# Kernel optimization log

Hardware: AMD Instinct MI355X
Metric: run time of the kernel (lower is better)

The kernel has to match this reference:

```python
import jax, jax.numpy as jnp
import numpy as np

N, E, F_IN, H, C = 10000, 320000, 256, 256, 40


def setup_inputs() -> dict:
    key = jax.random.key(0)
    ks = jax.random.split(key, 12)
    inp = {
        "x": jax.random.normal(ks[0], (N, F_IN), dtype=jnp.float32),
        "edge_index": jax.random.randint(ks[1], (2, E), 0, N, dtype=jnp.int64),
    }
    dims = [(F_IN, H), (H, H), (H, H), (H, H), (H, C)]
    for i, (din, dout) in enumerate(dims, start=1):
        scale = 1.0 / np.sqrt(din)
        inp[f"W{i}"] = jax.random.normal(ks[1 + i], (din, dout), dtype=jnp.float32) * scale
        inp[f"b{i}"] = jnp.zeros((dout,), dtype=jnp.float32)
    return inp


def _gcn_norm(edge_index, num_nodes, dtype):
    # GCNConv: add self-loops, symmetric normalization D^-1/2 (A+I) D^-1/2
    loops = jnp.arange(num_nodes, dtype=edge_index.dtype)
    src = jnp.concatenate([edge_index[0], loops])
    dst = jnp.concatenate([edge_index[1], loops])
    deg = jax.ops.segment_sum(jnp.ones_like(dst, dtype=dtype), dst, num_segments=num_nodes)
    dinv = jnp.where(deg > 0, deg ** -0.5, 0.0).astype(dtype)
    norm = dinv[src] * dinv[dst]  # [E+N]
    return src, dst, norm


def _conv(h, src, dst, norm, W, b, num_nodes):
    # linear transform then gather-scale-scatter aggregation
    h = h @ W                           # [N, dout]
    msg = h[src] * norm[:, None]        # [E+N, dout]
    return jax.ops.segment_sum(msg, dst, num_segments=num_nodes) + b


def reference(x, edge_index, W1, b1, W2, b2, W3, b3, W4, b4, W5, b5):
    num_nodes = x.shape[0]
    src, dst, norm = _gcn_norm(edge_index, num_nodes, x.dtype)
    h = jax.nn.relu(_conv(x, src, dst, norm, W1, b1, num_nodes))
    h = jax.nn.relu(_conv(h, src, dst, norm, W2, b2, num_nodes))
    h = jax.nn.relu(_conv(h, src, dst, norm, W3, b3, num_nodes))
    h = jax.nn.relu(_conv(h, src, dst, norm, W4, b4, num_nodes))
    logits = _conv(h, src, dst, norm, W5, b5, num_nodes)
    return jax.nn.log_softmax(logits, axis=1), logits
```

## Files before the change

### kernel.cpp

```cpp
#include <hip/hip_runtime.h>
#include <hip/hip_bf16.h>

#define N_NODES 10000
#define N_EDGES 320000
#define HDIM    256
#define NCLS    40

typedef __attribute__((ext_vector_type(8))) short short8;
typedef __attribute__((ext_vector_type(4))) float floatx4;
typedef unsigned long long ull;
typedef unsigned short ushort;

__device__ __forceinline__ float bf2f(ushort u) {
    union { unsigned int i; float f; } v; v.i = ((unsigned int)u) << 16; return v.f;
}
__device__ __forceinline__ ushort f2bf(float f) {
    __hip_bfloat16 h = __float2bfloat16(f);
    return *reinterpret_cast<ushort*>(&h);
}


__global__ void detect_kernel(const void* x, const void* ei, int* flags) {
    const int lane = threadIdx.x & 63;
    const ushort* u = (const ushort*)x;
    int e = (u[2 * lane] >> 7) & 0xFF;
    ull badmask = __ballot(e < 100 || e > 140);
    const int* ii = (const int*)ei;
    ull oddnz = __ballot(ii[2 * lane + 1] != 0);
    if (lane == 0) {
        flags[0] = (__popcll(badmask) >= 8) ? 1 : 0;
        flags[1] = (oddnz == 0) ? 1 : 0;
    }
}


struct PrepArgs {
    const void* x;
    const void* ei;
    const void* wsrc[10];
    ushort* wdst[10];
    int woffs[11];
    ushort* xb;
    int* src32;
    int* dst32;
    int* cnt;
    ushort* tbuf;
    ushort* hbuf;
    const int* flags;
};

#define PREP_XB 2500
#define PREP_WB 1069
#define PREP_EB 1250
#define PREP_ZB 40
#define PREP_SB 1
#define PREP_TOTAL (PREP_XB + PREP_WB + PREP_EB + PREP_ZB + PREP_SB)
#define WTOT 273448

__global__ __launch_bounds__(256)
void prep_kernel(PrepArgs a) {
    const int b = blockIdx.x;
    const int f32 = a.flags[0];
    if (b < PREP_XB) {
        int i4 = b * 256 + threadIdx.x;
        if (f32) {
            float4 v = ((const float4*)a.x)[i4];
            ull p = (ull)f2bf(v.x) | ((ull)f2bf(v.y) << 16) |
                    ((ull)f2bf(v.z) << 32) | ((ull)f2bf(v.w) << 48);
            ((ull*)a.xb)[i4] = p;
        } else {
            ((ull*)a.xb)[i4] = ((const ull*)a.x)[i4];
        }
    } else if (b < PREP_XB + PREP_WB) {
        int i = (b - PREP_XB) * 256 + threadIdx.x;
        if (i < WTOT) {
            int t = 0;
#pragma unroll
            for (int k = 1; k < 10; ++k) t += (i >= a.woffs[k]);
            int local = i - a.woffs[t];
            ushort v;
            if (f32) v = f2bf(((const float*)a.wsrc[t])[local]);
            else     v = ((const ushort*)a.wsrc[t])[local];
            a.wdst[t][local] = v;
        }
    } else if (b < PREP_XB + PREP_WB + PREP_EB) {
        int e = (b - PREP_XB - PREP_WB) * 256 + threadIdx.x;
        const int* ii = (const int*)a.ei;
        int s, d;
        if (a.flags[1]) { s = ii[2 * e]; d = ii[2 * (N_EDGES + e)]; }
        else            { s = ii[e];     d = ii[N_EDGES + e]; }
        a.src32[e] = ((unsigned)s < N_NODES) ? s : 0;
        a.dst32[e] = ((unsigned)d < N_NODES) ? d : 0;
    } else if (b < PREP_XB + PREP_WB + PREP_EB + PREP_ZB) {
        int i = (b - PREP_XB - PREP_WB - PREP_EB) * 256 + threadIdx.x;
        if (i < N_NODES) a.cnt[i] = 0;
    } else {
        int t = threadIdx.x;
        if (t < 64)       ((ull*)(a.tbuf + (size_t)N_NODES * 256))[t] = 0;
        else if (t < 128) ((ull*)(a.hbuf + (size_t)N_NODES * 256))[t - 64] = 0;
    }
}


__global__ void count_kernel(const int* __restrict__ dst, int* __restrict__ cnt) {
    int e = blockIdx.x * 256 + threadIdx.x;
    if (e < N_EDGES) atomicAdd(&cnt[dst[e]], 1);
}

__global__ __launch_bounds__(256)
void scan_dinv_kernel(const int* __restrict__ cnt, int* __restrict__ offs,
                      int* __restrict__ woff, float* __restrict__ dinv) {
    __shared__ int part[256];
    const int t = threadIdx.x;
    const int CH = 40;
    const int base = t * CH;
    int s = 0;
    for (int j = 0; j < CH; ++j) {
        int i = base + j;
        if (i < N_NODES) s += cnt[i];
    }
    part[t] = s;
    __syncthreads();
    for (int off = 1; off < 256; off <<= 1) {
        int v = (t >= off) ? part[t - off] : 0;
        __syncthreads();
        part[t] += v;
        __syncthreads();
    }
    int run = (t == 0) ? 0 : part[t - 1];
    for (int j = 0; j < CH; ++j) {
        int i = base + j;
        if (i < N_NODES) {
            int c = cnt[i];
            offs[i] = run;
            woff[i] = run;
            dinv[i] = rsqrtf((float)c + 1.0f);
            run += c;
        }
    }
}

__global__ void fill_kernel(const int* __restrict__ src, const int* __restrict__ dst,
                            int* __restrict__ woff, int* __restrict__ csr) {
    int e = blockIdx.x * 256 + threadIdx.x;
    if (e < N_EDGES) {
        int d = dst[e];
        int p = atomicAdd(&woff[d], 1);
        csr[p] = src[e];
    }
}


__global__ __launch_bounds__(256)
void gemm256_kernel(const ushort* __restrict__ A, const ushort* __restrict__ W,
                    const float* __restrict__ dinv, ushort* __restrict__ T) {
    const int lane = threadIdx.x & 63;
    const int wave = threadIdx.x >> 6;
    const int m = lane & 15;
    const int quad = lane >> 4;
    const int c0 = blockIdx.x * 32;

    short8 bfrag[2][8];
#pragma unroll
    for (int t = 0; t < 2; ++t)
#pragma unroll
        for (int s = 0; s < 8; ++s)
#pragma unroll
            for (int j = 0; j < 8; ++j)
                bfrag[t][s][j] = (short)W[(size_t)(s * 32 + quad * 8 + j) * 256 + c0 + t * 16 + m];

    const int step = gridDim.y * 4;
    for (int rt = blockIdx.y * 4 + wave; rt < N_NODES / 16; rt += step) {
        const int r0 = rt * 16;
        floatx4 acc0 = {0.f, 0.f, 0.f, 0.f};
        floatx4 acc1 = {0.f, 0.f, 0.f, 0.f};
        const ushort* arow = A + (size_t)(r0 + m) * 256 + quad * 8;
#pragma unroll
        for (int s = 0; s < 8; ++s) {
            short8 af = *(const short8*)(arow + s * 32);
            acc0 = __builtin_amdgcn_mfma_f32_16x16x32_bf16(af, bfrag[0][s], acc0, 0, 0, 0);
            acc1 = __builtin_amdgcn_mfma_f32_16x16x32_bf16(af, bfrag[1][s], acc1, 0, 0, 0);
        }
#pragma unroll
        for (int r = 0; r < 4; ++r) {
            int row = r0 + quad * 4 + r;
            float di = dinv[row];
            T[(size_t)row * 256 + c0 + m]      = f2bf(acc0[r] * di);
            T[(size_t)row * 256 + c0 + 16 + m] = f2bf(acc1[r] * di);
        }
    }
}


__global__ __launch_bounds__(256)
void gemm40_kernel(const ushort* __restrict__ A, const ushort* __restrict__ W,
                   const float* __restrict__ dinv, float* __restrict__ T) {
    const int lane = threadIdx.x & 63;
    const int wave = threadIdx.x >> 6;
    const int m = lane & 15;
    const int quad = lane >> 4;
    const int col = blockIdx.x * 16 + m;
    const bool colok = col < NCLS;

    short8 bfrag[8];
#pragma unroll
    for (int s = 0; s < 8; ++s)
#pragma unroll
        for (int j = 0; j < 8; ++j)
            bfrag[s][j] = colok ? (short)W[(size_t)(s * 32 + quad * 8 + j) * NCLS + col] : (short)0;

    const int step = gridDim.y * 4;
    for (int rt = blockIdx.y * 4 + wave; rt < N_NODES / 16; rt += step) {
        const int r0 = rt * 16;
        floatx4 acc = {0.f, 0.f, 0.f, 0.f};
        const ushort* arow = A + (size_t)(r0 + m) * 256 + quad * 8;
#pragma unroll
        for (int s = 0; s < 8; ++s) {
            short8 af = *(const short8*)(arow + s * 32);
            acc = __builtin_amdgcn_mfma_f32_16x16x32_bf16(af, bfrag[s], acc, 0, 0, 0);
        }
        if (colok) {
#pragma unroll
            for (int r = 0; r < 4; ++r) {
                int row = r0 + quad * 4 + r;
                T[(size_t)row * NCLS + col] = acc[r] * dinv[row];
            }
        }
    }
}


__device__ __forceinline__ void accum16(float* acc, int4 r) {
#pragma unroll
    for (int k = 0; k < 4; ++k) {
        union { int i; float f; } lo, hi;
        int d = (&r.x)[k];
        lo.i = d << 16;
        hi.i = d & 0xffff0000;
        acc[2 * k]     += lo.f;
        acc[2 * k + 1] += hi.f;
    }
}

__global__ __launch_bounds__(256)
void agg256_kernel(const ushort* __restrict__ T,
                   const int* __restrict__ csr, const int* __restrict__ offs,
                   const int* __restrict__ cnt, const float* __restrict__ dinv,
                   const ushort* __restrict__ bias,
                   ushort* __restrict__ H) {
    const int node = blockIdx.x * 4 + (threadIdx.x >> 6);
    const int lane = threadIdx.x & 63;
    const int qw = lane >> 4;
    const int q  = lane & 15;
    const int h  = blockIdx.y;
    const ushort* Tb = T + h * 128 + q * 8;
    const int start = offs[node];
    const int count = cnt[node];
    const float di = dinv[node];

    float acc[8];
    {
        int sinit = (qw == 0) ? node : N_NODES;
        int4 r = *(const int4*)(Tb + (size_t)sinit * 256);
#pragma unroll
        for (int k = 0; k < 4; ++k) {
            union { int i; float f; } lo, hi;
            int d = (&r.x)[k];
            lo.i = d << 16; hi.i = d & 0xffff0000;
            acc[2 * k] = lo.f; acc[2 * k + 1] = hi.f;
        }
    }

    for (int bj = 0; bj < count; bj += 64) {
        int mrem = count - bj;
        int mm = mrem < 64 ? mrem : 64;
        int idxv = (lane < mm) ? csr[start + bj + lane] : N_NODES;
        int j2 = 0;
        for (; j2 + 32 <= mm; j2 += 32) {
            int s[8];
#pragma unroll
            for (int k = 0; k < 8; ++k) s[k] = __shfl(idxv, j2 + 4 * k + qw);
            int4 r[8];
#pragma unroll
            for (int k = 0; k < 8; ++k) r[k] = *(const int4*)(Tb + (size_t)s[k] * 256);
#pragma unroll
            for (int k = 0; k < 8; ++k) accum16(acc, r[k]);
        }
        for (; j2 < mm; j2 += 4) {
            int sl = __shfl(idxv, (j2 + qw) & 63);
            int s = (j2 + qw < 64) ? sl : N_NODES;
            int4 r = *(const int4*)(Tb + (size_t)s * 256);
            accum16(acc, r);
        }
    }

#pragma unroll
    for (int i = 0; i < 8; ++i) {
        acc[i] += __shfl_xor(acc[i], 16);
        acc[i] += __shfl_xor(acc[i], 32);
    }

    if (qw == 0) {
        int4 bv = *(const int4*)(bias + h * 128 + q * 8);
        int out_d[4];
#pragma unroll
        for (int k = 0; k < 4; ++k) {
            union { int i; float f; } lo, hi;
            int d = (&bv.x)[k];
            lo.i = d << 16; hi.i = d & 0xffff0000;
            float v0 = fmaxf(acc[2 * k] * di + lo.f, 0.f);
            float v1 = fmaxf(acc[2 * k + 1] * di + hi.f, 0.f);
            out_d[k] = (int)f2bf(v0) | ((int)f2bf(v1) << 16);
        }
        *(int4*)(H + (size_t)node * 256 + h * 128 + q * 8) = *(int4*)out_d;
    }
}


__global__ __launch_bounds__(256)
void aggsoft_kernel(const float* __restrict__ T,
                    const int* __restrict__ csr, const int* __restrict__ offs,
                    const int* __restrict__ cnt, const float* __restrict__ dinv,
                    const ushort* __restrict__ bias,
                    void* __restrict__ out, const int* __restrict__ flags) {
    const int node = blockIdx.x * 4 + (threadIdx.x >> 6);
    const int lane = threadIdx.x & 63;
    const int start = offs[node];
    const int count = cnt[node];
    const float di = dinv[node];

    float acc = (lane < NCLS) ? T[(size_t)node * NCLS + lane] : 0.f;
    for (int bj = 0; bj < count; bj += 64) {
        int mrem = count - bj;
        int mm = mrem < 64 ? mrem : 64;
        int idxv = (lane < mm) ? csr[start + bj + lane] : 0;
        int jj = 0;
        for (; jj + 4 <= mm; jj += 4) {
            int s0 = __shfl(idxv, jj + 0);
            int s1 = __shfl(idxv, jj + 1);
            int s2 = __shfl(idxv, jj + 2);
            int s3 = __shfl(idxv, jj + 3);
            if (lane < NCLS) {
                float t0 = T[(size_t)s0 * NCLS + lane];
                float t1 = T[(size_t)s1 * NCLS + lane];
                float t2 = T[(size_t)s2 * NCLS + lane];
                float t3 = T[(size_t)s3 * NCLS + lane];
                acc += t0 + t1 + t2 + t3;
            }
        }
        for (; jj < mm; ++jj) {
            int s = __shfl(idxv, jj);
            if (lane < NCLS) acc += T[(size_t)s * NCLS + lane];
        }
    }

    float l = (lane < NCLS) ? (acc * di + bf2f(bias[lane])) : -INFINITY;
    float mx = l;
#pragma unroll
    for (int o = 32; o > 0; o >>= 1) mx = fmaxf(mx, __shfl_xor(mx, o));
    float e = (lane < NCLS) ? __expf(l - mx) : 0.f;
    float sum = e;
#pragma unroll
    for (int o = 32; o > 0; o >>= 1) sum += __shfl_xor(sum, o);
    float ls = l - mx - __logf(sum);
    if (lane < NCLS) {
        size_t i0 = (size_t)node * NCLS + lane;
        size_t i1 = (size_t)N_NODES * NCLS + i0;
        if (flags[0]) {
            ((float*)out)[i0] = ls;
            ((float*)out)[i1] = l;
        } else {
            ((ushort*)out)[i0] = f2bf(ls);
            ((ushort*)out)[i1] = f2bf(l);
        }
    }
}


static inline size_t alup(size_t x) { return (x + 255) & ~(size_t)255; }

extern "C" void kernel_launch(void* const* d_in, const int* in_sizes, int n_in,
                              void* d_out, int out_size, void* d_ws, size_t ws_size,
                              hipStream_t stream) {
    char* w = (char*)d_ws;
    int* flags   = (int*)w;           w += alup(16);
    float* dinv  = (float*)w;         w += alup(N_NODES * 4);
    int* cnt     = (int*)w;           w += alup(N_NODES * 4);
    int* offs    = (int*)w;           w += alup(N_NODES * 4);
    int* woff    = (int*)w;           w += alup(N_NODES * 4);
    int* src32   = (int*)w;           w += alup(N_EDGES * 4);
    int* dst32   = (int*)w;           w += alup(N_EDGES * 4);
    int* csr     = (int*)w;           w += alup(N_EDGES * 4);
    ushort* xb   = (ushort*)w;        w += alup((size_t)N_NODES * HDIM * 2);
    ushort* wb[5]; ushort* bb[5];
    for (int l = 0; l < 5; ++l) {
        int wn = (l < 4) ? HDIM * HDIM : HDIM * NCLS;
        int bn = (l < 4) ? HDIM : NCLS;
        wb[l] = (ushort*)w; w += alup((size_t)wn * 2);
        bb[l] = (ushort*)w; w += alup((size_t)bn * 2);
    }
    ushort* tbuf = (ushort*)w;        w += alup((size_t)(N_NODES + 16) * HDIM * 2);
    ushort* hbuf = (ushort*)w;        w += alup((size_t)(N_NODES + 16) * HDIM * 2);
    float* t5    = (float*)w;         w += alup((size_t)N_NODES * NCLS * 4);

    detect_kernel<<<1, 64, 0, stream>>>(d_in[0], d_in[1], flags);

    PrepArgs pa;
    pa.x = d_in[0];
    pa.ei = d_in[1];
    int sizes[10] = { HDIM * HDIM, HDIM, HDIM * HDIM, HDIM, HDIM * HDIM, HDIM,
                      HDIM * HDIM, HDIM, HDIM * NCLS, NCLS };
    int run = 0;
    for (int t = 0; t < 10; ++t) {
        pa.wsrc[t] = d_in[2 + t];
        pa.wdst[t] = (t & 1) ? bb[t >> 1] : wb[t >> 1];
        pa.woffs[t] = run;
        run += sizes[t];
    }
    pa.woffs[10] = run;
    pa.xb = xb; pa.src32 = src32; pa.dst32 = dst32; pa.cnt = cnt;
    pa.tbuf = tbuf; pa.hbuf = hbuf; pa.flags = flags;

    prep_kernel<<<PREP_TOTAL, 256, 0, stream>>>(pa);

    const int eblk = (N_EDGES + 255) / 256;
    count_kernel<<<eblk, 256, 0, stream>>>(dst32, cnt);
    scan_dinv_kernel<<<1, 256, 0, stream>>>(cnt, offs, woff, dinv);
    fill_kernel<<<eblk, 256, 0, stream>>>(src32, dst32, woff, csr);

    const int aggblk = N_NODES / 4;

    gemm256_kernel<<<dim3(8, 78), 256, 0, stream>>>(xb, wb[0], dinv, tbuf);
    agg256_kernel<<<dim3(aggblk, 2), 256, 0, stream>>>(tbuf, csr, offs, cnt, dinv, bb[0], hbuf);
    for (int l = 1; l < 4; ++l) {
        gemm256_kernel<<<dim3(8, 78), 256, 0, stream>>>(hbuf, wb[l], dinv, tbuf);
        agg256_kernel<<<dim3(aggblk, 2), 256, 0, stream>>>(tbuf, csr, offs, cnt, dinv, bb[l], hbuf);
    }
    gemm40_kernel<<<dim3(3, 80), 256, 0, stream>>>(hbuf, wb[4], dinv, t5);
    aggsoft_kernel<<<aggblk, 256, 0, stream>>>(t5, csr, offs, cnt, dinv, bb[4], d_out, flags);
}
```

Baseline: 316.6 us.

## Fuse degree counting into prep and aggregate full rows per wave

Removes the separate count kernel by doing the degree atomicAdd inside the edge-conversion blocks of prep. The detect kernel and the zeroing of cnt and buffer padding move into a single init kernel, so cnt is cleared before prep starts counting. The 256-wide aggregation now has each wave cover a full 512-byte row, with two half-waves processing alternating neighbors, replacing the two-block-column split. This halves the agg launch grid and the repeated CSR index reads, but gives each wave less neighbor parallelism per iteration.

```diff
diff --git a/kernel.cpp b/kernel.cpp
--- a/kernel.cpp
+++ b/kernel.cpp
@@ -20,16 +20,31 @@
 }
 
 
-__global__ void detect_kernel(const void* x, const void* ei, int* flags) {
-    const int lane = threadIdx.x & 63;
-    const ushort* u = (const ushort*)x;
-    int e = (u[2 * lane] >> 7) & 0xFF;
-    ull badmask = __ballot(e < 100 || e > 140);
-    const int* ii = (const int*)ei;
-    ull oddnz = __ballot(ii[2 * lane + 1] != 0);
-    if (lane == 0) {
-        flags[0] = (__popcll(badmask) >= 8) ? 1 : 0;
-        flags[1] = (oddnz == 0) ? 1 : 0;
+__global__ __launch_bounds__(256)
+void init_kernel(const void* x, const void* ei, int* flags, int* cnt,
+                 ushort* tbuf, ushort* hbuf) {
+    const int b = blockIdx.x;
+    const int tid = threadIdx.x;
+    if (b < 40) {
+        int i = b * 256 + tid;
+        if (i < N_NODES) cnt[i] = 0;
+    } else {
+        if (tid < 64) {
+            const int lane = tid;
+            const ushort* u = (const ushort*)x;
+            int e = (u[2 * lane] >> 7) & 0xFF;
+            ull badmask = __ballot(e < 100 || e > 140);
+            const int* ii = (const int*)ei;
+            ull oddnz = __ballot(ii[2 * lane + 1] != 0);
+            if (lane == 0) {
+                flags[0] = (__popcll(badmask) >= 8) ? 1 : 0;
+                flags[1] = (oddnz == 0) ? 1 : 0;
+            }
+        } else if (tid < 128) {
+            ((ull*)(tbuf + (size_t)N_NODES * 256))[tid - 64] = 0;
+        } else if (tid < 192) {
+            ((ull*)(hbuf + (size_t)N_NODES * 256))[tid - 128] = 0;
+        }
     }
 }
 
@@ -44,17 +59,13 @@
     int* src32;
     int* dst32;
     int* cnt;
-    ushort* tbuf;
-    ushort* hbuf;
     const int* flags;
 };
 
 #define PREP_XB 2500
 #define PREP_WB 1069
 #define PREP_EB 1250
-#define PREP_ZB 40
-#define PREP_SB 1
-#define PREP_TOTAL (PREP_XB + PREP_WB + PREP_EB + PREP_ZB + PREP_SB)
+#define PREP_TOTAL (PREP_XB + PREP_WB + PREP_EB)
 #define WTOT 273448
 
 __global__ __launch_bounds__(256)
@@ -83,29 +94,20 @@
             else     v = ((const ushort*)a.wsrc[t])[local];
             a.wdst[t][local] = v;
         }
-    } else if (b < PREP_XB + PREP_WB + PREP_EB) {
+    } else {
         int e = (b - PREP_XB - PREP_WB) * 256 + threadIdx.x;
         const int* ii = (const int*)a.ei;
         int s, d;
         if (a.flags[1]) { s = ii[2 * e]; d = ii[2 * (N_EDGES + e)]; }
         else            { s = ii[e];     d = ii[N_EDGES + e]; }
-        a.src32[e] = ((unsigned)s < N_NODES) ? s : 0;
-        a.dst32[e] = ((unsigned)d < N_NODES) ? d : 0;
-    } else if (b < PREP_XB + PREP_WB + PREP_EB + PREP_ZB) {
-        int i = (b - PREP_XB - PREP_WB - PREP_EB) * 256 + threadIdx.x;
-        if (i < N_NODES) a.cnt[i] = 0;
-    } else {
-        int t = threadIdx.x;
-        if (t < 64)       ((ull*)(a.tbuf + (size_t)N_NODES * 256))[t] = 0;
-        else if (t < 128) ((ull*)(a.hbuf + (size_t)N_NODES * 256))[t - 64] = 0;
-    }
-}
-
-
-__global__ void count_kernel(const int* __restrict__ dst, int* __restrict__ cnt) {
-    int e = blockIdx.x * 256 + threadIdx.x;
-    if (e < N_EDGES) atomicAdd(&cnt[dst[e]], 1);
-}
+        s = ((unsigned)s < N_NODES) ? s : 0;
+        d = ((unsigned)d < N_NODES) ? d : 0;
+        a.src32[e] = s;
+        a.dst32[e] = d;
+        atomicAdd(&a.cnt[d], 1);
+    }
+}
+
 
 __global__ __launch_bounds__(256)
 void scan_dinv_kernel(const int* __restrict__ cnt, int* __restrict__ offs,
@@ -140,6 +142,7 @@
     }
 }
 
+
 __global__ void fill_kernel(const int* __restrict__ src, const int* __restrict__ dst,
                             int* __restrict__ woff, int* __restrict__ csr) {
     int e = blockIdx.x * 256 + threadIdx.x;
@@ -250,18 +253,16 @@
                    ushort* __restrict__ H) {
     const int node = blockIdx.x * 4 + (threadIdx.x >> 6);
     const int lane = threadIdx.x & 63;
-    const int qw = lane >> 4;
-    const int q  = lane & 15;
-    const int h  = blockIdx.y;
-    const ushort* Tb = T + h * 128 + q * 8;
+    const int half = lane >> 5;
+    const int q = lane & 31;
     const int start = offs[node];
     const int count = cnt[node];
     const float di = dinv[node];
 
     float acc[8];
     {
-        int sinit = (qw == 0) ? node : N_NODES;
-        int4 r = *(const int4*)(Tb + (size_t)sinit * 256);
+        int sinit = half ? N_NODES : node;
+        int4 r = *(const int4*)(T + (size_t)sinit * 256 + q * 8);
 #pragma unroll
         for (int k = 0; k < 4; ++k) {
             union { int i; float f; } lo, hi;
@@ -276,32 +277,28 @@
         int mm = mrem < 64 ? mrem : 64;
         int idxv = (lane < mm) ? csr[start + bj + lane] : N_NODES;
         int j2 = 0;
-        for (; j2 + 32 <= mm; j2 += 32) {
+        for (; j2 + 16 <= mm; j2 += 16) {
             int s[8];
 #pragma unroll
-            for (int k = 0; k < 8; ++k) s[k] = __shfl(idxv, j2 + 4 * k + qw);
+            for (int k = 0; k < 8; ++k) s[k] = __shfl(idxv, j2 + 2 * k + half);
             int4 r[8];
 #pragma unroll
-            for (int k = 0; k < 8; ++k) r[k] = *(const int4*)(Tb + (size_t)s[k] * 256);
+            for (int k = 0; k < 8; ++k) r[k] = *(const int4*)(T + (size_t)s[k] * 256 + q * 8);
 #pragma unroll
             for (int k = 0; k < 8; ++k) accum16(acc, r[k]);
         }
-        for (; j2 < mm; j2 += 4) {
-            int sl = __shfl(idxv, (j2 + qw) & 63);
-            int s = (j2 + qw < 64) ? sl : N_NODES;
-            int4 r = *(const int4*)(Tb + (size_t)s * 256);
+        for (; j2 < mm; j2 += 2) {
+            int s = __shfl(idxv, j2 + half);
+            int4 r = *(const int4*)(T + (size_t)s * 256 + q * 8);
             accum16(acc, r);
         }
     }
 
 #pragma unroll
-    for (int i = 0; i < 8; ++i) {
-        acc[i] += __shfl_xor(acc[i], 16);
-        acc[i] += __shfl_xor(acc[i], 32);
-    }
-
-    if (qw == 0) {
-        int4 bv = *(const int4*)(bias + h * 128 + q * 8);
+    for (int i = 0; i < 8; ++i) acc[i] += __shfl_xor(acc[i], 32);
+
+    if (half == 0) {
+        int4 bv = *(const int4*)(bias + q * 8);
         int out_d[4];
 #pragma unroll
         for (int k = 0; k < 4; ++k) {
@@ -312,7 +309,7 @@
             float v1 = fmaxf(acc[2 * k + 1] * di + hi.f, 0.f);
             out_d[k] = (int)f2bf(v0) | ((int)f2bf(v1) << 16);
         }
-        *(int4*)(H + (size_t)node * 256 + h * 128 + q * 8) = *(int4*)out_d;
+        *(int4*)(H + (size_t)node * 256 + q * 8) = *(int4*)out_d;
     }
 }
 
@@ -403,7 +400,7 @@
     ushort* hbuf = (ushort*)w;        w += alup((size_t)(N_NODES + 16) * HDIM * 2);
     float* t5    = (float*)w;         w += alup((size_t)N_NODES * NCLS * 4);
 
-    detect_kernel<<<1, 64, 0, stream>>>(d_in[0], d_in[1], flags);
+    init_kernel<<<41, 256, 0, stream>>>(d_in[0], d_in[1], flags, cnt, tbuf, hbuf);
 
     PrepArgs pa;
     pa.x = d_in[0];
@@ -418,23 +415,20 @@
         run += sizes[t];
     }
     pa.woffs[10] = run;
-    pa.xb = xb; pa.src32 = src32; pa.dst32 = dst32; pa.cnt = cnt;
-    pa.tbuf = tbuf; pa.hbuf = hbuf; pa.flags = flags;
-
+    pa.xb = xb; pa.src32 = src32; pa.dst32 = dst32; pa.cnt = cnt; pa.flags = flags;
     prep_kernel<<<PREP_TOTAL, 256, 0, stream>>>(pa);
 
+    scan_dinv_kernel<<<1, 256, 0, stream>>>(cnt, offs, woff, dinv);
     const int eblk = (N_EDGES + 255) / 256;
-    count_kernel<<<eblk, 256, 0, stream>>>(dst32, cnt);
-    scan_dinv_kernel<<<1, 256, 0, stream>>>(cnt, offs, woff, dinv);
     fill_kernel<<<eblk, 256, 0, stream>>>(src32, dst32, woff, csr);
 
     const int aggblk = N_NODES / 4;
 
     gemm256_kernel<<<dim3(8, 78), 256, 0, stream>>>(xb, wb[0], dinv, tbuf);
-    agg256_kernel<<<dim3(aggblk, 2), 256, 0, stream>>>(tbuf, csr, offs, cnt, dinv, bb[0], hbuf);
+    agg256_kernel<<<aggblk, 256, 0, stream>>>(tbuf, csr, offs, cnt, dinv, bb[0], hbuf);
     for (int l = 1; l < 4; ++l) {
         gemm256_kernel<<<dim3(8, 78), 256, 0, stream>>>(hbuf, wb[l], dinv, tbuf);
-        agg256_kernel<<<dim3(aggblk, 2), 256, 0, stream>>>(tbuf, csr, offs, cnt, dinv, bb[l], hbuf);
+        agg256_kernel<<<aggblk, 256, 0, stream>>>(tbuf, csr, offs, cnt, dinv, bb[l], hbuf);
     }
     gemm40_kernel<<<dim3(3, 80), 256, 0, stream>>>(hbuf, wb[4], dinv, t5);
     aggsoft_kernel<<<aggblk, 256, 0, stream>>>(t5, csr, offs, cnt, dinv, bb[4], d_out, flags);
```

Measured after the change: 298.3 us. 5.8% less time.
